# Kernel optimization log

Hardware: AMD Instinct MI355X
Metric: run time of the kernel (lower is better)

## Reference

```python
import jax, jax.numpy as jnp
import numpy as np

N_IN, N_HIDDEN = 64, 1024
N, K = 8192, 16


def _linear_params(key, fan_in, fan_out):
    k1, k2 = jax.random.split(key)
    bound = 1.0 / np.sqrt(fan_in)
    W = jax.random.uniform(k1, (fan_in, fan_out), minval=-bound, maxval=bound, dtype=jnp.float32)
    b = jax.random.uniform(k2, (fan_out,), minval=-bound, maxval=bound, dtype=jnp.float32)
    return W, b


def setup_inputs() -> dict:
    key = jax.random.key(0)
    keys = jax.random.split(key, 7)
    towers = jax.random.normal(keys[0], (N, K, N_IN), dtype=jnp.float32)
    aggregate = jnp.zeros((1, N_HIDDEN), dtype=jnp.float32)
    MW1, Mb1 = _linear_params(keys[1], N_IN + N_HIDDEN, N_HIDDEN)
    MW2, Mb2 = _linear_params(keys[2], N_HIDDEN, N_HIDDEN)
    MW3, Mb3 = _linear_params(keys[3], N_HIDDEN, N_HIDDEN)
    OW1, Ob1 = _linear_params(keys[4], N_IN + N_HIDDEN, N_HIDDEN)
    OW2, Ob2 = _linear_params(keys[5], N_HIDDEN, N_HIDDEN)
    OW3, Ob3 = _linear_params(keys[6], N_HIDDEN, 1)
    return {"towers": towers, "aggregate": aggregate,
            "MW1": MW1, "Mb1": Mb1, "MW2": MW2, "Mb2": Mb2, "MW3": MW3, "Mb3": Mb3,
            "OW1": OW1, "Ob1": Ob1, "OW2": OW2, "Ob2": Ob2, "OW3": OW3, "Ob3": Ob3}


def reference(towers, aggregate, MW1, Mb1, MW2, Mb2, MW3, Mb3, OW1, Ob1, OW2, Ob2, OW3, Ob3):
    N_, K_, _ = towers.shape
    summary0 = jnp.broadcast_to(aggregate, (N_, aggregate.shape[1]))

    def step(summary, tower_k):
        # tower_k: (N, n_in); summary: (N, n_hidden)
        x = jnp.concatenate([summary, tower_k], axis=1)  # (N, n_hidden + n_in)
        h = jax.nn.relu(x @ OW1 + Ob1)
        h = jax.nn.relu(h @ OW2 + Ob2)
        pred = jax.nn.sigmoid(h @ OW3 + Ob3)[:, 0]  # (N,)
        m = jax.nn.relu(x @ MW1 + Mb1)
        m = jax.nn.relu(m @ MW2 + Mb2)
        m = jax.nn.relu(m @ MW3 + Mb3)
        return m, pred

    towers_k_first = jnp.transpose(towers, (1, 0, 2))  # (K, N, n_in)
    _, preds = jax.lax.scan(step, summary0, towers_k_first)  # preds: (K, N)
    return jnp.prod(preds, axis=0)  # (N,)
```

## Files before the change

kernel.cpp:

```cpp
#include <hip/hip_runtime.h>
#include <cstdint>
#include <cstddef>


typedef _Float16 f16x8 __attribute__((ext_vector_type(8)));
typedef float f32x16 __attribute__((ext_vector_type(16)));

#define MF(d, a, b) d = __builtin_amdgcn_mfma_f32_32x32x16_f16(a, b, d, 0, 0, 0)
#define CFENCE() asm volatile("" ::: "memory")

__device__ __forceinline__ void gload16(const void* g, void* l) {
  __builtin_amdgcn_global_load_lds(
      (__attribute__((address_space(1))) void*)const_cast<void*>(g),
      (__attribute__((address_space(3))) void*)l,
      16, 0, 0);
}

__global__ __launch_bounds__(256, 1)
void gemm_h_kernel(const _Float16* __restrict__ A0, int ldA0,
                   const _Float16* __restrict__ A1, int ldA1,
                   int kcut, int Ktot,
                   const _Float16* __restrict__ B,
                   const float* __restrict__ bias,
                   _Float16* __restrict__ C, int ldC,
                   const float* __restrict__ w3, float* __restrict__ sacc)
{
  __shared__ _Float16 sA[4][256 * 32];
  __shared__ _Float16 sB[4][128 * 32];

  const int lane = threadIdx.x & 63;
  const int wave = threadIdx.x >> 6;
  const int wm = (wave >> 1) * 128, wn = (wave & 1) * 64;
  const int mBase = blockIdx.x * 256, nBase = blockIdx.y * 128;

  const int lr  = 2 * (lane >> 3) + ((lane >> 2) & 1);
  const int lcs = (((lane & 3) ^ ((lane >> 3) & 3)) * 8);

  const int l31 = lane & 31, l5 = lane >> 5;
  const int rowoff = (l31 >> 1) * 64 + (l31 & 1) * 32;
  const int fswz = (l31 >> 1) & 3;
  const int ko0 = (l5 ^ fswz) * 8;
  const int ko1 = ((2 + l5) ^ fswz) * 8;

  const _Float16 *aS0[4], *aS1[4], *bS[2];
#pragma unroll
  for (int q = 0; q < 4; ++q) {
    const int row = mBase + (wave + q * 4) * 16 + lr;
    aS0[q] = A0 + (size_t)row * ldA0 + lcs;
    aS1[q] = A1 + (size_t)row * ldA1 + lcs;
  }
#pragma unroll
  for (int q = 0; q < 2; ++q) {
    const int row = nBase + (wave + q * 4) * 16 + lr;
    bS[q] = B + (size_t)row * Ktot + lcs;
  }

  f32x16 acc[4][2];
#pragma unroll
  for (int i = 0; i < 4; ++i)
#pragma unroll
    for (int j = 0; j < 2; ++j) acc[i][j] = (f32x16)0.0f;

  _Float16 *uA0 = &sA[0][0], *uA1 = &sA[1][0], *uA2 = &sA[2][0], *uA3 = &sA[3][0];
  _Float16 *uB0 = &sB[0][0], *uB1 = &sB[1][0], *uB2 = &sB[2][0], *uB3 = &sB[3][0];

  auto STAGE = [&](_Float16* dA, _Float16* dB, int kt) {
    const bool lo = kt < kcut;
    const int kl = lo ? kt : kt - kcut;
#pragma unroll
    for (int q = 0; q < 4; ++q)
      gload16((lo ? aS0[q] : aS1[q]) + kl, dA + (wave + q * 4) * 512);
#pragma unroll
    for (int q = 0; q < 2; ++q)
      gload16(bS[q] + kt, dB + (wave + q * 4) * 512);
  };

  auto DSREAD = [&](const _Float16* pA, const _Float16* pB,
                    f16x8 (&a)[4][2], f16x8 (&b)[2][2]) {
#pragma unroll
    for (int i = 0; i < 4; ++i) {
      const int base = (wm + i * 32) * 32 + rowoff;
      a[i][0] = *(const f16x8*)(pA + base + ko0);
      a[i][1] = *(const f16x8*)(pA + base + ko1);
    }
#pragma unroll
    for (int j = 0; j < 2; ++j) {
      const int base = (wn + j * 32) * 32 + rowoff;
      b[j][0] = *(const f16x8*)(pB + base + ko0);
      b[j][1] = *(const f16x8*)(pB + base + ko1);
    }
  };

  auto MFMACL = [&](f16x8 (&a)[4][2], f16x8 (&b)[2][2]) {
#pragma unroll
    for (int kh = 0; kh < 2; ++kh)
#pragma unroll
      for (int i = 0; i < 4; ++i)
#pragma unroll
        for (int j = 0; j < 2; ++j) MF(acc[i][j], a[i][kh], b[j][kh]);
  };

  f16x8 aX[4][2], bX[2][2];
  f16x8 aY[4][2], bY[2][2];

  const int NT = Ktot >> 5;
  STAGE(uA0, uB0, 0);
  STAGE(uA1, uB1, 32);
  asm volatile("s_waitcnt vmcnt(6)" ::: "memory");
  __builtin_amdgcn_s_barrier();
  CFENCE();
  DSREAD(uA0, uB0, aX, bX);

  for (int t = 0; t < NT; t += 2) {
    {
      const bool s2 = (t + 2) < NT;
      if (s2) STAGE(uA2, uB2, (t + 2) * 32);
      if (s2) asm volatile("s_waitcnt vmcnt(6)" ::: "memory");
      else    asm volatile("s_waitcnt vmcnt(0)" ::: "memory");
      __builtin_amdgcn_s_barrier();
      CFENCE();
      asm volatile("s_waitcnt lgkmcnt(0)" ::: "memory");
      DSREAD(uA1, uB1, aY, bY);
      __builtin_amdgcn_sched_barrier(0);
      __builtin_amdgcn_s_setprio(1);
      MFMACL(aX, bX);
      __builtin_amdgcn_s_setprio(0);
    }
    {
      const bool s2 = (t + 3) < NT;
      const bool r2 = (t + 2) < NT;
      if (s2) STAGE(uA3, uB3, (t + 3) * 32);
      if (s2)      asm volatile("s_waitcnt vmcnt(6)" ::: "memory");
      else if (r2) asm volatile("s_waitcnt vmcnt(0)" ::: "memory");
      __builtin_amdgcn_s_barrier();
      CFENCE();
      asm volatile("s_waitcnt lgkmcnt(0)" ::: "memory");
      if (r2) DSREAD(uA2, uB2, aX, bX);
      __builtin_amdgcn_sched_barrier(0);
      __builtin_amdgcn_s_setprio(1);
      MFMACL(aY, bY);
      __builtin_amdgcn_s_setprio(0);
    }
    { _Float16* tp;
      tp = uA0; uA0 = uA2; uA2 = tp;  tp = uA1; uA1 = uA3; uA3 = tp;
      tp = uB0; uB0 = uB2; uB2 = tp;  tp = uB1; uB1 = uB3; uB3 = tp; }
  }

  float bv[2], w3v[2];
#pragma unroll
  for (int j = 0; j < 2; ++j) {
    const int col = nBase + wn + j * 32 + l31;
    bv[j] = bias[col];
    w3v[j] = sacc ? w3[col] : 0.0f;
  }

  if (sacc) {
#pragma unroll
    for (int i = 0; i < 4; ++i)
#pragma unroll
      for (int r = 0; r < 16; ++r) {
        float pr = 0.0f;
#pragma unroll
        for (int j = 0; j < 2; ++j)
          pr += fmaxf(acc[i][j][r] + bv[j], 0.0f) * w3v[j];
        pr += __shfl_xor(pr, 1);
        pr += __shfl_xor(pr, 2);
        pr += __shfl_xor(pr, 4);
        pr += __shfl_xor(pr, 8);
        pr += __shfl_xor(pr, 16);
        if (l31 == 0)
          atomicAdd(&sacc[mBase + wm + i * 32 + (r & 3) + 8 * (r >> 2) + 4 * l5], pr);
      }
  } else {
#pragma unroll
    for (int i = 0; i < 4; ++i)
#pragma unroll
      for (int j = 0; j < 2; ++j)
#pragma unroll
        for (int r = 0; r < 16; ++r) {
          const int row = mBase + wm + i * 32 + (r & 3) + 8 * (r >> 2) + 4 * l5;
          const int col = nBase + wn + j * 32 + l31;
          float v = fmaxf(acc[i][j][r] + bv[j], 0.0f);
          C[(size_t)row * ldC + col] = (_Float16)v;
        }
  }
}

__global__ void wconv_kernel(const float* __restrict__ W, int K, int N,
                             _Float16* __restrict__ oH) {
  int idx = blockIdx.x * 256 + threadIdx.x;
  if (idx >= K * N) return;
  int n = idx / K, k = idx - n * K;
  oH[idx] = (_Float16)W[(size_t)k * N + n];
}

__global__ void init_summary_kernel(const float* __restrict__ agg,
                                    _Float16* __restrict__ sH,
                                    float* __restrict__ sacc) {
  int idx = blockIdx.x * 256 + threadIdx.x;
  sH[idx] = (_Float16)agg[idx & 1023];
  if (idx < 8192) sacc[idx] = 0.0f;
}

__global__ void biascat_kernel(const float* __restrict__ b0,
                               const float* __restrict__ b1,
                               float* __restrict__ o) {
  int idx = blockIdx.x * 256 + threadIdx.x;
  o[idx] = (idx < 1024) ? b0[idx] : b1[idx - 1024];
}

__global__ void tow_conv_all_kernel(const float* __restrict__ towers,
                                    _Float16* __restrict__ oH) {
  size_t idx = (size_t)blockIdx.x * 256 + threadIdx.x;
  int f = idx & 63;
  int n = (int)((idx >> 6) & 8191);
  int k = (int)(idx >> 19);
  oH[idx] = (_Float16)towers[((size_t)n * 16 + k) * 64 + f];
}

__global__ void pred_final_kernel(float* __restrict__ sacc, const float* __restrict__ b3,
                                  float* __restrict__ out, int step) {
  int row = blockIdx.x * 256 + threadIdx.x;
  float p = 1.0f / (1.0f + expf(-(sacc[row] + b3[0])));
  out[row] = (step == 0) ? p : out[row] * p;
  sacc[row] = 0.0f;
}

extern "C" void kernel_launch(void* const* d_in, const int* in_sizes, int n_in,
                              void* d_out, int out_size, void* d_ws, size_t ws_size,
                              hipStream_t stream) {
  const float* towers = (const float*)d_in[0];
  const float* agg    = (const float*)d_in[1];
  const float* MW1 = (const float*)d_in[2];
  const float* Mb1 = (const float*)d_in[3];
  const float* MW2 = (const float*)d_in[4];
  const float* Mb2 = (const float*)d_in[5];
  const float* MW3 = (const float*)d_in[6];
  const float* Mb3 = (const float*)d_in[7];
  const float* OW1 = (const float*)d_in[8];
  const float* Ob1 = (const float*)d_in[9];
  const float* OW2 = (const float*)d_in[10];
  const float* Ob2 = (const float*)d_in[11];
  const float* OW3 = (const float*)d_in[12];
  const float* Ob3 = (const float*)d_in[13];
  float* out = (float*)d_out;

  _Float16* p = (_Float16*)d_ws;
  _Float16* W1catH = p; p += (size_t)2048 * 1088;
  _Float16* MW2tH  = p; p += (size_t)1024 * 1024;
  _Float16* OW2tH  = p; p += (size_t)1024 * 1024;
  _Float16* MW3tH  = p; p += (size_t)1024 * 1024;
  _Float16* sumH   = p; p += (size_t)8192 * 1024;
  _Float16* mh1    = p; p += (size_t)8192 * 2048;
  _Float16* m2H    = p; p += (size_t)8192 * 1024;
  _Float16* towAllH = p; p += (size_t)16 * 8192 * 64;
  float* sacc  = (float*)p;
  float* b1cat = sacc + 8192;

  {
    int tot = 1088 * 1024;
    wconv_kernel<<<dim3((tot + 255) / 256), dim3(256), 0, stream>>>(MW1, 1088, 1024, W1catH);
    wconv_kernel<<<dim3((tot + 255) / 256), dim3(256), 0, stream>>>(OW1, 1088, 1024, W1catH + (size_t)1024 * 1088);
    tot = 1024 * 1024;
    wconv_kernel<<<dim3((tot + 255) / 256), dim3(256), 0, stream>>>(MW2, 1024, 1024, MW2tH);
    wconv_kernel<<<dim3((tot + 255) / 256), dim3(256), 0, stream>>>(OW2, 1024, 1024, OW2tH);
    wconv_kernel<<<dim3((tot + 255) / 256), dim3(256), 0, stream>>>(MW3, 1024, 1024, MW3tH);
    biascat_kernel<<<dim3(8), dim3(256), 0, stream>>>(Mb1, Ob1, b1cat);
    init_summary_kernel<<<dim3(32768), dim3(256), 0, stream>>>(agg, sumH, sacc);
    tow_conv_all_kernel<<<dim3(32768), dim3(256), 0, stream>>>(towers, towAllH);
  }

  const dim3 G1(32, 16), G(32, 8), B256(256);
  for (int k = 0; k < 16; ++k) {
    const _Float16* towH = towAllH + (size_t)k * 8192 * 64;

    gemm_h_kernel<<<G1, B256, 0, stream>>>(sumH, 1024, towH, 64, 1024, 1088,
                                           W1catH, b1cat, mh1, 2048, nullptr, nullptr);
    gemm_h_kernel<<<G, B256, 0, stream>>>(mh1, 2048, mh1, 2048, 1024, 1024,
                                          MW2tH, Mb2, m2H, 1024, nullptr, nullptr);
    gemm_h_kernel<<<G, B256, 0, stream>>>(mh1 + 1024, 2048, mh1 + 1024, 2048, 1024, 1024,
                                          OW2tH, Ob2, nullptr, 1024, OW3, sacc);
    gemm_h_kernel<<<G, B256, 0, stream>>>(m2H, 1024, m2H, 1024, 1024, 1024,
                                          MW3tH, Mb3, sumH, 1024, nullptr, nullptr);
    pred_final_kernel<<<dim3(32), dim3(256), 0, stream>>>(sacc, Ob3, out, k);
  }
}
```

Before: 2.453 ms.

## Deepen GEMM LDS pipeline from four to five buffers with prefetch distance three

Grows the shared-memory ring from four to five stages and issues global-to-LDS loads three K-tiles ahead instead of two, rotating buffer pointers each half-iteration. The wait counts are relaxed so more loads stay in flight while MFMAs run, to hide more global memory latency. It costs 25% more LDS (about 120KB per block), which could limit occupancy or run close to the LDS capacity. It also makes the vmcnt bookkeeping at the tail more complex.

```diff
diff --git a/kernel.cpp b/kernel.cpp
--- a/kernel.cpp
+++ b/kernel.cpp
@@ -25,8 +25,8 @@
                    _Float16* __restrict__ C, int ldC,
                    const float* __restrict__ w3, float* __restrict__ sacc)
 {
-  __shared__ _Float16 sA[4][256 * 32];
-  __shared__ _Float16 sB[4][128 * 32];
+  __shared__ _Float16 sA[5][256 * 32];
+  __shared__ _Float16 sB[5][128 * 32];
 
   const int lane = threadIdx.x & 63;
   const int wave = threadIdx.x >> 6;
@@ -61,8 +61,10 @@
 #pragma unroll
     for (int j = 0; j < 2; ++j) acc[i][j] = (f32x16)0.0f;
 
-  _Float16 *uA0 = &sA[0][0], *uA1 = &sA[1][0], *uA2 = &sA[2][0], *uA3 = &sA[3][0];
-  _Float16 *uB0 = &sB[0][0], *uB1 = &sB[1][0], *uB2 = &sB[2][0], *uB3 = &sB[3][0];
+  _Float16 *qA0 = &sA[0][0], *qA1 = &sA[1][0], *qA2 = &sA[2][0],
+           *qA3 = &sA[3][0], *qA4 = &sA[4][0];
+  _Float16 *qB0 = &sB[0][0], *qB1 = &sB[1][0], *qB2 = &sB[2][0],
+           *qB3 = &sB[3][0], *qB4 = &sB[4][0];
 
   auto STAGE = [&](_Float16* dA, _Float16* dB, int kt) {
     const bool lo = kt < kcut;
@@ -100,50 +102,59 @@
         for (int j = 0; j < 2; ++j) MF(acc[i][j], a[i][kh], b[j][kh]);
   };
 
+  auto ROT = [&]() {
+    _Float16* tp;
+    tp = qA0; qA0 = qA1; qA1 = qA2; qA2 = qA3; qA3 = qA4; qA4 = tp;
+    tp = qB0; qB0 = qB1; qB1 = qB2; qB2 = qB3; qB3 = qB4; qB4 = tp;
+  };
+
   f16x8 aX[4][2], bX[2][2];
   f16x8 aY[4][2], bY[2][2];
 
   const int NT = Ktot >> 5;
-  STAGE(uA0, uB0, 0);
-  STAGE(uA1, uB1, 32);
-  asm volatile("s_waitcnt vmcnt(6)" ::: "memory");
+  STAGE(qA0, qB0, 0);
+  STAGE(qA1, qB1, 32);
+  STAGE(qA2, qB2, 64);
+  asm volatile("s_waitcnt vmcnt(12)" ::: "memory");
   __builtin_amdgcn_s_barrier();
   CFENCE();
-  DSREAD(uA0, uB0, aX, bX);
+  DSREAD(qA0, qB0, aX, bX);
 
   for (int t = 0; t < NT; t += 2) {
     {
-      const bool s2 = (t + 2) < NT;
-      if (s2) STAGE(uA2, uB2, (t + 2) * 32);
-      if (s2) asm volatile("s_waitcnt vmcnt(6)" ::: "memory");
-      else    asm volatile("s_waitcnt vmcnt(0)" ::: "memory");
+      const bool s = (t + 3) < NT;
+      if (s) STAGE(qA3, qB3, (t + 3) * 32);
+      if (s)                 asm volatile("s_waitcnt vmcnt(12)" ::: "memory");
+      else if ((t + 2) < NT) asm volatile("s_waitcnt vmcnt(6)"  ::: "memory");
+      else                   asm volatile("s_waitcnt vmcnt(0)"  ::: "memory");
       __builtin_amdgcn_s_barrier();
       CFENCE();
       asm volatile("s_waitcnt lgkmcnt(0)" ::: "memory");
-      DSREAD(uA1, uB1, aY, bY);
+      DSREAD(qA1, qB1, aY, bY);
       __builtin_amdgcn_sched_barrier(0);
       __builtin_amdgcn_s_setprio(1);
       MFMACL(aX, bX);
       __builtin_amdgcn_s_setprio(0);
+      ROT();
     }
     {
-      const bool s2 = (t + 3) < NT;
-      const bool r2 = (t + 2) < NT;
-      if (s2) STAGE(uA3, uB3, (t + 3) * 32);
-      if (s2)      asm volatile("s_waitcnt vmcnt(6)" ::: "memory");
-      else if (r2) asm volatile("s_waitcnt vmcnt(0)" ::: "memory");
+      const int u = t + 1;
+      const bool s = (u + 3) < NT;
+      const bool r = (u + 1) < NT;
+      if (s) STAGE(qA3, qB3, (u + 3) * 32);
+      if (s)                 asm volatile("s_waitcnt vmcnt(12)" ::: "memory");
+      else if ((u + 2) < NT) asm volatile("s_waitcnt vmcnt(6)"  ::: "memory");
+      else if (r)            asm volatile("s_waitcnt vmcnt(0)"  ::: "memory");
       __builtin_amdgcn_s_barrier();
       CFENCE();
       asm volatile("s_waitcnt lgkmcnt(0)" ::: "memory");
-      if (r2) DSREAD(uA2, uB2, aX, bX);
+      if (r) DSREAD(qA1, qB1, aX, bX);
       __builtin_amdgcn_sched_barrier(0);
       __builtin_amdgcn_s_setprio(1);
       MFMACL(aY, bY);
       __builtin_amdgcn_s_setprio(0);
-    }
-    { _Float16* tp;
-      tp = uA0; uA0 = uA2; uA2 = tp;  tp = uA1; uA1 = uA3; uA3 = tp;
-      tp = uB0; uB0 = uB2; uB2 = tp;  tp = uB1; uB1 = uB3; uB3 = tp; }
+      ROT();
+    }
   }
 
   float bv[2], w3v[2];
```

Result: no change. 2.455 ms (+0.1%).

## Switch GEMM to 128x128 single-buffered tiles with higher occupancy

Applied to the files above, without the earlier changes.

Replaces the 256x128 tile GEMM, with its explicit four-stage LDS pipeline, by a 128x128 tile that loads a 64-wide K slice each iteration behind plain barriers. The launch grid doubles and launch bounds allow three blocks per CU, so latency is meant to be hidden by occupancy rather than software pipelining. The smaller tiles reduce per-block register and LDS use. In exchange, operand reuse per tile drops and load/compute overlap within a block is lost.

```diff
diff --git a/kernel.cpp b/kernel.cpp
--- a/kernel.cpp
+++ b/kernel.cpp
@@ -5,9 +5,6 @@
 
 typedef _Float16 f16x8 __attribute__((ext_vector_type(8)));
 typedef float f32x16 __attribute__((ext_vector_type(16)));
-
-#define MF(d, a, b) d = __builtin_amdgcn_mfma_f32_32x32x16_f16(a, b, d, 0, 0, 0)
-#define CFENCE() asm volatile("" ::: "memory")
 
 __device__ __forceinline__ void gload16(const void* g, void* l) {
   __builtin_amdgcn_global_load_lds(
@@ -16,7 +13,7 @@
       16, 0, 0);
 }
 
-__global__ __launch_bounds__(256, 1)
+__global__ __launch_bounds__(256, 3)
 void gemm_h_kernel(const _Float16* __restrict__ A0, int ldA0,
                    const _Float16* __restrict__ A1, int ldA1,
                    int kcut, int Ktot,
@@ -25,125 +22,59 @@
                    _Float16* __restrict__ C, int ldC,
                    const float* __restrict__ w3, float* __restrict__ sacc)
 {
-  __shared__ _Float16 sA[4][256 * 32];
-  __shared__ _Float16 sB[4][128 * 32];
+  __shared__ _Float16 sAh[128 * 64];
+  __shared__ _Float16 sBh[128 * 64];
 
   const int lane = threadIdx.x & 63;
   const int wave = threadIdx.x >> 6;
-  const int wm = (wave >> 1) * 128, wn = (wave & 1) * 64;
-  const int mBase = blockIdx.x * 256, nBase = blockIdx.y * 128;
-
-  const int lr  = 2 * (lane >> 3) + ((lane >> 2) & 1);
-  const int lcs = (((lane & 3) ^ ((lane >> 3) & 3)) * 8);
+  const int wm = (wave >> 1) * 64, wn = (wave & 1) * 64;
+  const int mBase = blockIdx.x * 128, nBase = blockIdx.y * 128;
+
+  const int lr = lane >> 3;
+  const int lcs8 = ((lane & 7) ^ lr) * 8;
 
   const int l31 = lane & 31, l5 = lane >> 5;
-  const int rowoff = (l31 >> 1) * 64 + (l31 & 1) * 32;
-  const int fswz = (l31 >> 1) & 3;
-  const int ko0 = (l5 ^ fswz) * 8;
-  const int ko1 = ((2 + l5) ^ fswz) * 8;
-
-  const _Float16 *aS0[4], *aS1[4], *bS[2];
-#pragma unroll
-  for (int q = 0; q < 4; ++q) {
-    const int row = mBase + (wave + q * 4) * 16 + lr;
-    aS0[q] = A0 + (size_t)row * ldA0 + lcs;
-    aS1[q] = A1 + (size_t)row * ldA1 + lcs;
-  }
-#pragma unroll
-  for (int q = 0; q < 2; ++q) {
-    const int row = nBase + (wave + q * 4) * 16 + lr;
-    bS[q] = B + (size_t)row * Ktot + lcs;
-  }
-
-  f32x16 acc[4][2];
-#pragma unroll
-  for (int i = 0; i < 4; ++i)
-#pragma unroll
-    for (int j = 0; j < 2; ++j) acc[i][j] = (f32x16)0.0f;
-
-  _Float16 *uA0 = &sA[0][0], *uA1 = &sA[1][0], *uA2 = &sA[2][0], *uA3 = &sA[3][0];
-  _Float16 *uB0 = &sB[0][0], *uB1 = &sB[1][0], *uB2 = &sB[2][0], *uB3 = &sB[3][0];
-
-  auto STAGE = [&](_Float16* dA, _Float16* dB, int kt) {
-    const bool lo = kt < kcut;
-    const int kl = lo ? kt : kt - kcut;
-#pragma unroll
-    for (int q = 0; q < 4; ++q)
-      gload16((lo ? aS0[q] : aS1[q]) + kl, dA + (wave + q * 4) * 512);
-#pragma unroll
-    for (int q = 0; q < 2; ++q)
-      gload16(bS[q] + kt, dB + (wave + q * 4) * 512);
-  };
-
-  auto DSREAD = [&](const _Float16* pA, const _Float16* pB,
-                    f16x8 (&a)[4][2], f16x8 (&b)[2][2]) {
-#pragma unroll
-    for (int i = 0; i < 4; ++i) {
-      const int base = (wm + i * 32) * 32 + rowoff;
-      a[i][0] = *(const f16x8*)(pA + base + ko0);
-      a[i][1] = *(const f16x8*)(pA + base + ko1);
+  const int fswz = l31 & 7;
+
+  f32x16 acc[2][2];
+#pragma unroll
+  for (int i = 0; i < 2; ++i)
+#pragma unroll
+    for (int j = 0; j < 2; ++j)
+      acc[i][j] = (f32x16)0.0f;
+
+  for (int kt = 0; kt < Ktot; kt += 64) {
+    const _Float16* aH; int pA, kl;
+    if (kt < kcut) { aH = A0; pA = ldA0; kl = kt; }
+    else           { aH = A1; pA = ldA1; kl = kt - kcut; }
+
+#pragma unroll
+    for (int cc = 0; cc < 4; ++cc) {
+      const int c = wave * 4 + cc;
+      const int arow = mBase + c * 8 + lr;
+      const int brow = nBase + c * 8 + lr;
+      gload16(aH + (size_t)arow * pA   + kl + lcs8, &sAh[c * 512]);
+      gload16(B  + (size_t)brow * Ktot + kt + lcs8, &sBh[c * 512]);
     }
-#pragma unroll
-    for (int j = 0; j < 2; ++j) {
-      const int base = (wn + j * 32) * 32 + rowoff;
-      b[j][0] = *(const f16x8*)(pB + base + ko0);
-      b[j][1] = *(const f16x8*)(pB + base + ko1);
+    __syncthreads();
+
+#pragma unroll
+    for (int kh = 0; kh < 4; ++kh) {
+      const int ko = ((kh * 2 + l5) ^ fswz) * 8;
+      f16x8 ah[2], bh[2];
+#pragma unroll
+      for (int i = 0; i < 2; ++i)
+        ah[i] = *(const f16x8*)&sAh[(wm + i * 32 + l31) * 64 + ko];
+#pragma unroll
+      for (int j = 0; j < 2; ++j)
+        bh[j] = *(const f16x8*)&sBh[(wn + j * 32 + l31) * 64 + ko];
+#pragma unroll
+      for (int i = 0; i < 2; ++i)
+#pragma unroll
+        for (int j = 0; j < 2; ++j)
+          acc[i][j] = __builtin_amdgcn_mfma_f32_32x32x16_f16(ah[i], bh[j], acc[i][j], 0, 0, 0);
     }
-  };
-
-  auto MFMACL = [&](f16x8 (&a)[4][2], f16x8 (&b)[2][2]) {
-#pragma unroll
-    for (int kh = 0; kh < 2; ++kh)
-#pragma unroll
-      for (int i = 0; i < 4; ++i)
-#pragma unroll
-        for (int j = 0; j < 2; ++j) MF(acc[i][j], a[i][kh], b[j][kh]);
-  };
-
-  f16x8 aX[4][2], bX[2][2];
-  f16x8 aY[4][2], bY[2][2];
-
-  const int NT = Ktot >> 5;
-  STAGE(uA0, uB0, 0);
-  STAGE(uA1, uB1, 32);
-  asm volatile("s_waitcnt vmcnt(6)" ::: "memory");
-  __builtin_amdgcn_s_barrier();
-  CFENCE();
-  DSREAD(uA0, uB0, aX, bX);
-
-  for (int t = 0; t < NT; t += 2) {
-    {
-      const bool s2 = (t + 2) < NT;
-      if (s2) STAGE(uA2, uB2, (t + 2) * 32);
-      if (s2) asm volatile("s_waitcnt vmcnt(6)" ::: "memory");
-      else    asm volatile("s_waitcnt vmcnt(0)" ::: "memory");
-      __builtin_amdgcn_s_barrier();
-      CFENCE();
-      asm volatile("s_waitcnt lgkmcnt(0)" ::: "memory");
-      DSREAD(uA1, uB1, aY, bY);
-      __builtin_amdgcn_sched_barrier(0);
-      __builtin_amdgcn_s_setprio(1);
-      MFMACL(aX, bX);
-      __builtin_amdgcn_s_setprio(0);
-    }
-    {
-      const bool s2 = (t + 3) < NT;
-      const bool r2 = (t + 2) < NT;
-      if (s2) STAGE(uA3, uB3, (t + 3) * 32);
-      if (s2)      asm volatile("s_waitcnt vmcnt(6)" ::: "memory");
-      else if (r2) asm volatile("s_waitcnt vmcnt(0)" ::: "memory");
-      __builtin_amdgcn_s_barrier();
-      CFENCE();
-      asm volatile("s_waitcnt lgkmcnt(0)" ::: "memory");
-      if (r2) DSREAD(uA2, uB2, aX, bX);
-      __builtin_amdgcn_sched_barrier(0);
-      __builtin_amdgcn_s_setprio(1);
-      MFMACL(aY, bY);
-      __builtin_amdgcn_s_setprio(0);
-    }
-    { _Float16* tp;
-      tp = uA0; uA0 = uA2; uA2 = tp;  tp = uA1; uA1 = uA3; uA3 = tp;
-      tp = uB0; uB0 = uB2; uB2 = tp;  tp = uB1; uB1 = uB3; uB3 = tp; }
+    __syncthreads();
   }
 
   float bv[2], w3v[2];
@@ -156,7 +87,7 @@
 
   if (sacc) {
 #pragma unroll
-    for (int i = 0; i < 4; ++i)
+    for (int i = 0; i < 2; ++i)
 #pragma unroll
       for (int r = 0; r < 16; ++r) {
         float pr = 0.0f;
@@ -173,7 +104,7 @@
       }
   } else {
 #pragma unroll
-    for (int i = 0; i < 4; ++i)
+    for (int i = 0; i < 2; ++i)
 #pragma unroll
       for (int j = 0; j < 2; ++j)
 #pragma unroll
@@ -270,7 +201,7 @@
     tow_conv_all_kernel<<<dim3(32768), dim3(256), 0, stream>>>(towers, towAllH);
   }
 
-  const dim3 G1(32, 16), G(32, 8), B256(256);
+  const dim3 G1(64, 16), G(64, 8), B256(256);
   for (int k = 0; k < 16; ++k) {
     const _Float16* towH = towAllH + (size_t)k * 8192 * 64;
 
```

Result: faster. 2.107 ms (-14.1%).
